# Optimization experiments

Measured on AMD Instinct MI355X. Metric: run time of the kernel, lower is better.

The kernel has to match this reference:

```python
import jax, jax.numpy as jnp
import numpy as np

B, L, C, OUT = 8, 256, 512, 512


def setup_inputs() -> dict:
    key = jax.random.key(0)
    ks = jax.random.split(key, 8)
    xd = jax.random.normal(ks[0], (B, L, C), jnp.float32)
    xt = jax.random.normal(ks[1], (B, L, C), jnp.float32)
    # Linear weights stored (in, out): y = x @ W + b (equiv. to torch x @ W^T)
    Wc = jax.random.normal(ks[2], (C, C), jnp.float32) * 0.02
    bc = jnp.zeros((C,), jnp.float32)
    Wp = jax.random.normal(ks[3], (C, C), jnp.float32) * 0.02
    bp = jnp.zeros((C,), jnp.float32)
    Wf = jax.random.normal(ks[4], (C, OUT), jnp.float32) * 0.02
    bf = jnp.zeros((OUT,), jnp.float32)
    return {"xd": xd, "xt": xt, "Wc": Wc, "bc": bc, "Wp": Wp, "bp": bp, "Wf": Wf, "bf": bf}


def reference(xd, xt, Wc, bc, Wp, bp, Wf, bf):
    # projected features
    pt = jax.nn.relu(xt) @ Wp + bp              # (b, Lt, C)
    pc = jax.nn.relu(xd) @ Wc + bc              # (b, Ld, C)
    # sigmoid bilinear scores: (b, Lt, Ld) == (b, Ld, Lt) since Lt == Ld structurally
    scores = jax.nn.sigmoid(jnp.einsum('bic,bkc->bik', pt, pc))
    # normalize by total per-batch sum
    w = scores / jnp.sum(scores, axis=(1, 2), keepdims=True)
    # tanh of elementwise outer product, reduced with attention weights
    # cp[b,c] = sum_{i,j} tanh(xd[b,i,c] * xt[b,j,c]) * w[b,i,j]
    cp = jnp.einsum('bijc,bij->bc', jnp.tanh(xd[:, :, None, :] * xt[:, None, :, :]), w)
    return cp @ Wf + bf
```

## Files before the change

### kernel.cpp

```cpp
#include <hip/hip_runtime.h>
#include <math.h>

#define B_   8
#define L_   256
#define C_   512
#define OUT_ 512

typedef _Float16 half8 __attribute__((ext_vector_type(8)));
typedef _Float16 half4 __attribute__((ext_vector_type(4)));
typedef float    f32x4 __attribute__((ext_vector_type(4)));
typedef float    f32x2 __attribute__((ext_vector_type(2)));

__global__ __launch_bounds__(256)
void proj_mfma_kernel(const float* __restrict__ xt, const float* __restrict__ Wp,
                      const float* __restrict__ bp,
                      const float* __restrict__ xd, const float* __restrict__ Wc,
                      const float* __restrict__ bc,
                      _Float16* __restrict__ pt, _Float16* __restrict__ pc)
{
    const int which = blockIdx.z;
    const float* __restrict__ X    = which ? xd : xt;
    const float* __restrict__ W    = which ? Wc : Wp;
    const float* __restrict__ bias = which ? bc : bp;
    _Float16*    __restrict__ Y    = which ? pc : pt;

    __shared__ _Float16 Ah[2][64][40];
    __shared__ _Float16 Bh[2][64][40];
    __shared__ _Float16 Ot[64][72];

    const int tid = threadIdx.x;
    const int m0 = blockIdx.y << 6, n0 = blockIdx.x << 6;
    const int lane = tid & 63, wv = tid >> 6;
    const int l15 = lane & 15, quad = lane >> 4;

    const int srow = tid >> 2, sch = (tid & 3) << 3;
    const float* Ag = X + (size_t)(m0 + srow) * C_ + sch;
    const int nl = tid & 63, kseg = tid >> 6;
    const float* Bg = W + (size_t)(kseg << 3) * C_ + n0 + nl;

    float4 a0 = *(const float4*)(Ag);
    float4 a1 = *(const float4*)(Ag + 4);
    float wr[8];
    #pragma unroll
    for (int r = 0; r < 8; ++r) wr[r] = Bg[(size_t)r * C_];

    {
        half8 av;
        av[0] = (_Float16)fmaxf(a0.x, 0.f); av[1] = (_Float16)fmaxf(a0.y, 0.f);
        av[2] = (_Float16)fmaxf(a0.z, 0.f); av[3] = (_Float16)fmaxf(a0.w, 0.f);
        av[4] = (_Float16)fmaxf(a1.x, 0.f); av[5] = (_Float16)fmaxf(a1.y, 0.f);
        av[6] = (_Float16)fmaxf(a1.z, 0.f); av[7] = (_Float16)fmaxf(a1.w, 0.f);
        *(half8*)&Ah[0][srow][sch] = av;
        half8 bv;
        #pragma unroll
        for (int r = 0; r < 8; ++r) bv[r] = (_Float16)wr[r];
        *(half8*)&Bh[0][nl][kseg << 3] = bv;
    }

    f32x4 acc[4] = {};
    for (int ks = 0; ks < 16; ++ks) {
        const int cur = ks & 1;
        if (ks < 15) {
            Ag += 32;
            Bg += 32 * C_;
            a0 = *(const float4*)(Ag);
            a1 = *(const float4*)(Ag + 4);
            #pragma unroll
            for (int r = 0; r < 8; ++r) wr[r] = Bg[(size_t)r * C_];
        }
        __syncthreads();
        half8 af = *(const half8*)&Ah[cur][(wv << 4) + l15][quad << 3];
        #pragma unroll
        for (int nb = 0; nb < 4; ++nb) {
            half8 bf = *(const half8*)&Bh[cur][(nb << 4) + l15][quad << 3];
            acc[nb] = __builtin_amdgcn_mfma_f32_16x16x32_f16(af, bf, acc[nb], 0, 0, 0);
        }
        if (ks < 15) {
            half8 av;
            av[0] = (_Float16)fmaxf(a0.x, 0.f); av[1] = (_Float16)fmaxf(a0.y, 0.f);
            av[2] = (_Float16)fmaxf(a0.z, 0.f); av[3] = (_Float16)fmaxf(a0.w, 0.f);
            av[4] = (_Float16)fmaxf(a1.x, 0.f); av[5] = (_Float16)fmaxf(a1.y, 0.f);
            av[6] = (_Float16)fmaxf(a1.z, 0.f); av[7] = (_Float16)fmaxf(a1.w, 0.f);
            *(half8*)&Ah[cur ^ 1][srow][sch] = av;
            half8 bv;
            #pragma unroll
            for (int r = 0; r < 8; ++r) bv[r] = (_Float16)wr[r];
            *(half8*)&Bh[cur ^ 1][nl][kseg << 3] = bv;
        }
    }

    __syncthreads();
    #pragma unroll
    for (int nb = 0; nb < 4; ++nb) {
        const float bz = bias[n0 + (nb << 4) + l15];
        #pragma unroll
        for (int r = 0; r < 4; ++r)
            Ot[(wv << 4) + (quad << 2) + r][(nb << 4) + l15] = (_Float16)(acc[nb][r] + bz);
    }
    __syncthreads();
    const int erow = tid >> 3, ech = (tid & 7) << 3;
    #pragma unroll
    for (int h = 0; h < 64; h += 32)
        *(half8*)&Y[(size_t)(m0 + erow + h) * C_ + n0 + ech] = *(const half8*)&Ot[erow + h][ech];
}

__device__ __forceinline__ float sigmoid_fast(float z) {
    float e = __builtin_amdgcn_exp2f(-1.4426950408889634f * z);
    return __builtin_amdgcn_rcpf(e + 1.0f);
}

__global__ __launch_bounds__(256)
void scores_kernel(const _Float16* __restrict__ pt, const _Float16* __restrict__ pc,
                   float* __restrict__ w, float* __restrict__ sums_part)
{
    const int bx = blockIdx.x, by = blockIdx.y, b = blockIdx.z;
    const int i0 = bx << 5, j0 = by << 5;
    const int tid = threadIdx.x;
    const int lane = tid & 63, wv = tid >> 6;
    const int l15 = lane & 15, quad = lane >> 4;
    const int mq = wv >> 1, nq = wv & 1;

    __shared__ float wred[4];

    const _Float16* __restrict__ Ap =
        pt + (size_t)(b * L_ + i0 + mq * 16 + l15) * C_ + (quad << 3);
    const _Float16* __restrict__ Bp =
        pc + (size_t)(b * L_ + j0 + nq * 16 + l15) * C_ + (quad << 3);

    f32x4 acc = {};
    #pragma unroll
    for (int ks = 0; ks < 16; ++ks) {
        half8 af = *(const half8*)(Ap + (ks << 5));
        half8 bf = *(const half8*)(Bp + (ks << 5));
        acc = __builtin_amdgcn_mfma_f32_16x16x32_f16(af, bf, acc, 0, 0, 0);
    }

    float4 sg;
    sg.x = sigmoid_fast(acc[0]);
    sg.y = sigmoid_fast(acc[1]);
    sg.z = sigmoid_fast(acc[2]);
    sg.w = sigmoid_fast(acc[3]);

    float* __restrict__ wp =
        w + (size_t)(b * L_ + i0 + mq * 16 + (quad << 2)) * L_ + j0 + nq * 16 + l15;
    wp[0 * L_] = sg.x;
    wp[1 * L_] = sg.y;
    wp[2 * L_] = sg.z;
    wp[3 * L_] = sg.w;

    float lsum = (sg.x + sg.y) + (sg.z + sg.w);
    #pragma unroll
    for (int off = 32; off; off >>= 1) lsum += __shfl_xor(lsum, off);
    if (lane == 0) wred[wv] = lsum;
    __syncthreads();
    if (tid == 0)
        sums_part[(b << 6) | (bx << 3) | by] = (wred[0] + wred[1]) + (wred[2] + wred[3]);
}

__global__ __launch_bounds__(512, 8)
void tanh_cp_kernel(const float* __restrict__ w, const float* __restrict__ xd,
                    const float* __restrict__ xt, float* __restrict__ partials)
{
    const int bx = blockIdx.x, by = blockIdx.y, b = blockIdx.z;
    const int i0 = bx << 4, j0 = by << 4;
    const int tid = threadIdx.x;

    __shared__ float ws_[16][20];

    if (tid < 64) {
        const int ir = tid >> 2, j4 = (tid & 3) << 2;
        const float4 v = *(const float4*)(w + (size_t)(b * L_ + i0 + ir) * L_ + j0 + j4);
        ws_[j4 + 0][ir] = v.x;
        ws_[j4 + 1][ir] = v.y;
        ws_[j4 + 2][ir] = v.z;
        ws_[j4 + 3][ir] = v.w;
    }

    const int c = tid;
    const float* __restrict__ xdb = xd + (size_t)(b * L_ + i0) * C_ + c;
    const float* __restrict__ xtb = xt + (size_t)(b * L_ + j0) * C_ + c;

    f32x2 xds2[8];
    #pragma unroll
    for (int i = 0; i < 8; ++i) {
        xds2[i].x = xdb[(size_t)(2 * i) * C_];
        xds2[i].y = xdb[(size_t)(2 * i + 1) * C_];
    }

    __syncthreads();

    f32x2 acc01 = {0.f, 0.f}, acc23 = {0.f, 0.f};
    #pragma unroll
    for (int jj = 0; jj < 16; ++jj) {
        const float xv = xtb[(size_t)jj * C_] * 2.8853900817779268f;
        #pragma unroll
        for (int i = 0; i < 16; i += 4) {
            const float4 w4 = *(const float4*)&ws_[jj][i];
            f32x2 x01 = xds2[i >> 1] * xv;
            f32x2 e01 = { __builtin_amdgcn_exp2f(x01.x), __builtin_amdgcn_exp2f(x01.y) };
            f32x2 q01 = e01 + 1.0f;
            float rp01 = __builtin_amdgcn_rcpf(q01.x * q01.y);
            f32x2 r01 = rp01 * __builtin_shufflevector(q01, q01, 1, 0);
            f32x2 w01 = { w4.x, w4.y };
            acc01 = w01 * r01 + acc01;
            f32x2 x23 = xds2[(i >> 1) + 1] * xv;
            f32x2 e23 = { __builtin_amdgcn_exp2f(x23.x), __builtin_amdgcn_exp2f(x23.y) };
            f32x2 q23 = e23 + 1.0f;
            float rp23 = __builtin_amdgcn_rcpf(q23.x * q23.y);
            f32x2 r23 = rp23 * __builtin_shufflevector(q23, q23, 1, 0);
            f32x2 w23 = { w4.z, w4.w };
            acc23 = w23 * r23 + acc23;
        }
    }
    const int p = (bx << 4) | by;
    partials[(size_t)((b << 8) | p) * C_ + c] =
        (acc01.x + acc01.y) + (acc23.x + acc23.y);
}

__global__ __launch_bounds__(512)
void finalize_kernel(const float* __restrict__ partials, const float* __restrict__ sums_part,
                     const float* __restrict__ Wf, const float* __restrict__ bfv,
                     float* __restrict__ out)
{
    const int b = blockIdx.y;
    const int t = threadIdx.x;
    __shared__ float cp[C_];
    __shared__ float red[512];
    __shared__ float sumsh;

    red[t] = (t < 64) ? sums_part[(b << 6) | t] : 0.f;

    float s = 0.f;
    #pragma unroll 8
    for (int p = 0; p < 256; ++p)
        s += partials[(size_t)((b << 8) | p) * C_ + t];

    __syncthreads();
    for (int st = 256; st > 0; st >>= 1) {
        if (t < st) red[t] += red[t + st];
        __syncthreads();
    }
    if (t == 0) sumsh = red[0];
    __syncthreads();

    cp[t] = 1.0f - 2.0f * s / sumsh;
    __syncthreads();

    const int o  = ((int)blockIdx.x << 6) | (t & 63);
    const int c0 = (t >> 6) << 6;
    float acc = 0.f;
    #pragma unroll 8
    for (int i = 0; i < 64; ++i) {
        const int cc = c0 + i;
        acc = fmaf(cp[cc], Wf[(size_t)cc * OUT_ + o], acc);
    }
    red[t] = acc;
    __syncthreads();
    if (t < 64) {
        float a = 0.f;
        #pragma unroll
        for (int g = 0; g < 8; ++g) a += red[(g << 6) | t];
        out[(size_t)b * OUT_ + o] = a + bfv[o];
    }
}

extern "C" void kernel_launch(void* const* d_in, const int* in_sizes, int n_in,
                              void* d_out, int out_size, void* d_ws, size_t ws_size,
                              hipStream_t stream)
{
    const float* xd = (const float*)d_in[0];
    const float* xt = (const float*)d_in[1];
    const float* Wc = (const float*)d_in[2];
    const float* bc = (const float*)d_in[3];
    const float* Wp = (const float*)d_in[4];
    const float* bp = (const float*)d_in[5];
    const float* Wf = (const float*)d_in[6];
    const float* bf = (const float*)d_in[7];
    float* out = (float*)d_out;

    _Float16* pt = (_Float16*)d_ws;
    _Float16* pc = pt + 1048576;
    float* w         = (float*)(pc + 1048576);
    float* partials  = w + 524288;
    float* sums_part = partials + 1048576;

    proj_mfma_kernel<<<dim3(8, 32, 2), 256, 0, stream>>>(xt, Wp, bp, xd, Wc, bc, pt, pc);
    scores_kernel<<<dim3(8, 8, 8), 256, 0, stream>>>(pt, pc, w, sums_part);
    tanh_cp_kernel<<<dim3(16, 16, 8), 512, 0, stream>>>(w, xd, xt, partials);
    finalize_kernel<<<dim3(8, 8), 512, 0, stream>>>(partials, sums_part, Wf, bf, out);
}
```

Measured before the change: 151.6 us.

## Fuse sigmoid score computation into tanh reduction kernel and enlarge tiles

Drops the separate scores kernel. Each tanh/cp block now computes its own 16x32 tile of sigmoid scores with split-K MFMA, reduced through shared memory, then runs the tanh-weighted accumulation over 32 xt rows instead of 16. This removes one launch and the round trip of the score matrix through global memory, and halves the number of partial sums the finalize kernel reads. The cost is a larger per-block register footprint (32 cached xt values) and fewer blocks (1024 instead of 2048), which may lower occupancy under the launch bound.

Result: slower. 156.5 us (+3.3%).

```diff
diff --git a/kernel.cpp b/kernel.cpp
--- a/kernel.cpp
+++ b/kernel.cpp
@@ -109,158 +109,141 @@
     return __builtin_amdgcn_rcpf(e + 1.0f);
 }
 
-__global__ __launch_bounds__(256)
-void scores_kernel(const _Float16* __restrict__ pt, const _Float16* __restrict__ pc,
-                   float* __restrict__ w, float* __restrict__ sums_part)
-{
-    const int bx = blockIdx.x, by = blockIdx.y, b = blockIdx.z;
-    const int i0 = bx << 5, j0 = by << 5;
+__global__ __launch_bounds__(512, 8)
+void cp_tanh_kernel(const _Float16* __restrict__ pt, const _Float16* __restrict__ pc,
+                    const float* __restrict__ xd, const float* __restrict__ xt,
+                    float* __restrict__ cpart, float* __restrict__ tile_sum)
+{
+    const int rm = blockIdx.x;
+    const int b  = blockIdx.y;
+    const int i0 = (rm >> 3) << 4;
+    const int j0 = (rm & 7) << 5;
     const int tid = threadIdx.x;
-    const int lane = tid & 63, wv = tid >> 6;
+    const int wv = tid >> 6, lane = tid & 63;
     const int l15 = lane & 15, quad = lane >> 4;
-    const int mq = wv >> 1, nq = wv & 1;
-
-    __shared__ float wred[4];
-
-    const _Float16* __restrict__ Ap =
-        pt + (size_t)(b * L_ + i0 + mq * 16 + l15) * C_ + (quad << 3);
-    const _Float16* __restrict__ Bp =
-        pc + (size_t)(b * L_ + j0 + nq * 16 + l15) * C_ + (quad << 3);
-
-    f32x4 acc = {};
-    #pragma unroll
-    for (int ks = 0; ks < 16; ++ks) {
-        half8 af = *(const half8*)(Ap + (ks << 5));
-        half8 bf = *(const half8*)(Bp + (ks << 5));
-        acc = __builtin_amdgcn_mfma_f32_16x16x32_f16(af, bf, acc, 0, 0, 0);
-    }
-
-    float4 sg;
-    sg.x = sigmoid_fast(acc[0]);
-    sg.y = sigmoid_fast(acc[1]);
-    sg.z = sigmoid_fast(acc[2]);
-    sg.w = sigmoid_fast(acc[3]);
-
-    float* __restrict__ wp =
-        w + (size_t)(b * L_ + i0 + mq * 16 + (quad << 2)) * L_ + j0 + nq * 16 + l15;
-    wp[0 * L_] = sg.x;
-    wp[1 * L_] = sg.y;
-    wp[2 * L_] = sg.z;
-    wp[3 * L_] = sg.w;
-
-    float lsum = (sg.x + sg.y) + (sg.z + sg.w);
-    #pragma unroll
-    for (int off = 32; off; off >>= 1) lsum += __shfl_xor(lsum, off);
-    if (lane == 0) wred[wv] = lsum;
-    __syncthreads();
-    if (tid == 0)
-        sums_part[(b << 6) | (bx << 3) | by] = (wred[0] + wred[1]) + (wred[2] + wred[3]);
-}
-
-__global__ __launch_bounds__(512, 8)
-void tanh_cp_kernel(const float* __restrict__ w, const float* __restrict__ xd,
-                    const float* __restrict__ xt, float* __restrict__ partials)
-{
-    const int bx = blockIdx.x, by = blockIdx.y, b = blockIdx.z;
-    const int i0 = bx << 4, j0 = by << 4;
-    const int tid = threadIdx.x;
-
-    __shared__ float ws_[16][20];
-
-    if (tid < 64) {
-        const int ir = tid >> 2, j4 = (tid & 3) << 2;
-        const float4 v = *(const float4*)(w + (size_t)(b * L_ + i0 + ir) * L_ + j0 + j4);
-        ws_[j4 + 0][ir] = v.x;
-        ws_[j4 + 1][ir] = v.y;
-        ws_[j4 + 2][ir] = v.z;
-        ws_[j4 + 3][ir] = v.w;
-    }
-
-    const int c = tid;
-    const float* __restrict__ xdb = xd + (size_t)(b * L_ + i0) * C_ + c;
-    const float* __restrict__ xtb = xt + (size_t)(b * L_ + j0) * C_ + c;
-
+
+    __shared__ float red[8][256];
+    __shared__ float ws[2][16][20];
+    __shared__ float wred[8];
+
+    const float* __restrict__ xdb = xd + (size_t)(b * L_ + i0) * C_ + tid;
+    const float* __restrict__ xtb = xt + (size_t)(b * L_ + j0) * C_ + tid;
     f32x2 xds2[8];
     #pragma unroll
-    for (int i = 0; i < 8; ++i) {
-        xds2[i].x = xdb[(size_t)(2 * i) * C_];
-        xds2[i].y = xdb[(size_t)(2 * i + 1) * C_];
-    }
-
-    __syncthreads();
+    for (int h = 0; h < 8; ++h) {
+        xds2[h].x = xdb[(size_t)(2 * h) * C_]     * 2.8853900817779268f;
+        xds2[h].y = xdb[(size_t)(2 * h + 1) * C_] * 2.8853900817779268f;
+    }
+    float xtv[32];
+    #pragma unroll
+    for (int j = 0; j < 32; ++j) xtv[j] = xtb[(size_t)j * C_];
+
+    {
+        const int jh = wv & 1, kq = wv >> 1;
+        const _Float16* __restrict__ Ap =
+            pt + (size_t)(b * L_ + i0 + l15) * C_ + (kq << 7) + (quad << 3);
+        const _Float16* __restrict__ Bp =
+            pc + (size_t)(b * L_ + j0 + (jh << 4) + l15) * C_ + (kq << 7) + (quad << 3);
+        f32x4 acc = {};
+        #pragma unroll
+        for (int ks = 0; ks < 4; ++ks) {
+            half8 af = *(const half8*)(Ap + (ks << 5));
+            half8 bf = *(const half8*)(Bp + (ks << 5));
+            acc = __builtin_amdgcn_mfma_f32_16x16x32_f16(af, bf, acc, 0, 0, 0);
+        }
+        *(f32x4*)&red[wv][lane << 2] = acc;
+    }
+    __syncthreads();
+    {
+        const int jh2 = tid >> 8, slot = tid & 255;
+        const float sc = (red[jh2][slot]     + red[jh2 + 2][slot]) +
+                         (red[jh2 + 4][slot] + red[jh2 + 6][slot]);
+        const float z = sigmoid_fast(sc);
+        const int ln = slot >> 2, r = slot & 3;
+        ws[jh2][ln & 15][((ln >> 4) << 2) + r] = z;
+        float lsum = z;
+        #pragma unroll
+        for (int off = 32; off; off >>= 1) lsum += __shfl_xor(lsum, off);
+        if (lane == 0) wred[wv] = lsum;
+    }
+    __syncthreads();
+    if (tid == 0) {
+        float ts = 0.f;
+        #pragma unroll
+        for (int v = 0; v < 8; ++v) ts += wred[v];
+        tile_sum[(b << 7) | rm] = ts;
+    }
 
     f32x2 acc01 = {0.f, 0.f}, acc23 = {0.f, 0.f};
     #pragma unroll
-    for (int jj = 0; jj < 16; ++jj) {
-        const float xv = xtb[(size_t)jj * C_] * 2.8853900817779268f;
-        #pragma unroll
-        for (int i = 0; i < 16; i += 4) {
-            const float4 w4 = *(const float4*)&ws_[jj][i];
-            f32x2 x01 = xds2[i >> 1] * xv;
-            f32x2 e01 = { __builtin_amdgcn_exp2f(x01.x), __builtin_amdgcn_exp2f(x01.y) };
-            f32x2 q01 = e01 + 1.0f;
-            float rp01 = __builtin_amdgcn_rcpf(q01.x * q01.y);
-            f32x2 r01 = rp01 * __builtin_shufflevector(q01, q01, 1, 0);
-            f32x2 w01 = { w4.x, w4.y };
-            acc01 = w01 * r01 + acc01;
-            f32x2 x23 = xds2[(i >> 1) + 1] * xv;
-            f32x2 e23 = { __builtin_amdgcn_exp2f(x23.x), __builtin_amdgcn_exp2f(x23.y) };
-            f32x2 q23 = e23 + 1.0f;
-            float rp23 = __builtin_amdgcn_rcpf(q23.x * q23.y);
-            f32x2 r23 = rp23 * __builtin_shufflevector(q23, q23, 1, 0);
-            f32x2 w23 = { w4.z, w4.w };
-            acc23 = w23 * r23 + acc23;
-        }
-    }
-    const int p = (bx << 4) | by;
-    partials[(size_t)((b << 8) | p) * C_ + c] =
+    for (int jh = 0; jh < 2; ++jh) {
+        #pragma unroll
+        for (int jj = 0; jj < 16; ++jj) {
+            const float xv = xtv[(jh << 4) + jj];
+            #pragma unroll
+            for (int iq = 0; iq < 4; ++iq) {
+                const float4 w4 = *(const float4*)&ws[jh][jj][iq << 2];
+                f32x2 x01 = xds2[iq * 2] * xv;
+                f32x2 e01 = { __builtin_amdgcn_exp2f(x01.x), __builtin_amdgcn_exp2f(x01.y) };
+                f32x2 q01 = e01 + 1.0f;
+                float rp01 = __builtin_amdgcn_rcpf(q01.x * q01.y);
+                f32x2 r01 = rp01 * __builtin_shufflevector(q01, q01, 1, 0);
+                f32x2 w01 = { w4.x, w4.y };
+                acc01 = w01 * r01 + acc01;
+                f32x2 x23 = xds2[iq * 2 + 1] * xv;
+                f32x2 e23 = { __builtin_amdgcn_exp2f(x23.x), __builtin_amdgcn_exp2f(x23.y) };
+                f32x2 q23 = e23 + 1.0f;
+                float rp23 = __builtin_amdgcn_rcpf(q23.x * q23.y);
+                f32x2 r23 = rp23 * __builtin_shufflevector(q23, q23, 1, 0);
+                f32x2 w23 = { w4.z, w4.w };
+                acc23 = w23 * r23 + acc23;
+            }
+        }
+    }
+    cpart[(size_t)((b << 7) | rm) * C_ + tid] =
         (acc01.x + acc01.y) + (acc23.x + acc23.y);
 }
 
 __global__ __launch_bounds__(512)
-void finalize_kernel(const float* __restrict__ partials, const float* __restrict__ sums_part,
+void finalize_kernel(const float* __restrict__ cpart, const float* __restrict__ tile_sum,
                      const float* __restrict__ Wf, const float* __restrict__ bfv,
                      float* __restrict__ out)
 {
-    const int b = blockIdx.y;
-    const int t = threadIdx.x;
+    const int oc = blockIdx.x, b = blockIdx.y;
+    const int tid = threadIdx.x;
     __shared__ float cp[C_];
-    __shared__ float red[512];
-    __shared__ float sumsh;
-
-    red[t] = (t < 64) ? sums_part[(b << 6) | t] : 0.f;
+    __shared__ float redf[512];
 
     float s = 0.f;
     #pragma unroll 8
-    for (int p = 0; p < 256; ++p)
-        s += partials[(size_t)((b << 8) | p) * C_ + t];
-
-    __syncthreads();
-    for (int st = 256; st > 0; st >>= 1) {
-        if (t < st) red[t] += red[t + st];
+    for (int rm = 0; rm < 128; ++rm)
+        s += cpart[(size_t)((b << 7) + rm) * C_ + tid];
+
+    if (tid < 128) redf[tid] = tile_sum[(b << 7) + tid];
+    __syncthreads();
+    for (int st = 64; st > 0; st >>= 1) {
+        if (tid < st) redf[tid] += redf[tid + st];
         __syncthreads();
     }
-    if (t == 0) sumsh = red[0];
-    __syncthreads();
-
-    cp[t] = 1.0f - 2.0f * s / sumsh;
-    __syncthreads();
-
-    const int o  = ((int)blockIdx.x << 6) | (t & 63);
-    const int c0 = (t >> 6) << 6;
+    const float S = redf[0];
+    cp[tid] = 1.0f - 2.0f * s / S;
+    __syncthreads();
+
+    const int o  = (oc << 6) | (tid & 63);
+    const int c0 = (tid >> 6) << 6;
     float acc = 0.f;
     #pragma unroll 8
     for (int i = 0; i < 64; ++i) {
         const int cc = c0 + i;
         acc = fmaf(cp[cc], Wf[(size_t)cc * OUT_ + o], acc);
     }
-    red[t] = acc;
-    __syncthreads();
-    if (t < 64) {
+    redf[tid] = acc;
+    __syncthreads();
+    if (tid < 64) {
         float a = 0.f;
         #pragma unroll
-        for (int g = 0; g < 8; ++g) a += red[(g << 6) | t];
-        out[(size_t)b * OUT_ + o] = a + bfv[o];
+        for (int g = 0; g < 8; ++g) a += redf[(g << 6) | tid];
+        out[(size_t)b * OUT_ + ((oc << 6) | tid)] = a + bfv[(oc << 6) | tid];
     }
 }
 
@@ -268,6 +251,7 @@
                               void* d_out, int out_size, void* d_ws, size_t ws_size,
                               hipStream_t stream)
 {
+    (void)in_sizes; (void)n_in; (void)out_size; (void)ws_size;
     const float* xd = (const float*)d_in[0];
     const float* xt = (const float*)d_in[1];
     const float* Wc = (const float*)d_in[2];
@@ -280,12 +264,10 @@
 
     _Float16* pt = (_Float16*)d_ws;
     _Float16* pc = pt + 1048576;
-    float* w         = (float*)(pc + 1048576);
-    float* partials  = w + 524288;
-    float* sums_part = partials + 1048576;
+    float* cpart    = (float*)(pc + 1048576);
+    float* tile_sum = cpart + 524288;
 
     proj_mfma_kernel<<<dim3(8, 32, 2), 256, 0, stream>>>(xt, Wp, bp, xd, Wc, bc, pt, pc);
-    scores_kernel<<<dim3(8, 8, 8), 256, 0, stream>>>(pt, pc, w, sums_part);
-    tanh_cp_kernel<<<dim3(16, 16, 8), 512, 0, stream>>>(w, xd, xt, partials);
-    finalize_kernel<<<dim3(8, 8), 512, 0, stream>>>(partials, sums_part, Wf, bf, out);
-}
+    cp_tanh_kernel<<<dim3(128, 8), 512, 0, stream>>>(pt, pc, xd, xt, cpart, tile_sum);
+    finalize_kernel<<<dim3(8, 8), 512, 0, stream>>>(cpart, tile_sum, Wf, bf, out);
+}
```
